# Performance work log

Measured on AMD Instinct MI355X. Metric: run time of the kernel, lower is better.

The kernel has to match this reference:

```python
import jax, jax.numpy as jnp
import numpy as np

B, L_TEXT, N_TOKEN = 8, 2048, 2048
C_TEXT, C_OUT = 3584, 384
C_HID = C_OUT * 2
CHAIN_TYPES = (1, 2)   # heavy, light
CDR_TYPES = (2, 4, 6)  # CDR1/2/3


def setup_inputs() -> dict:
    key = jax.random.key(0)
    ks = jax.random.split(key, 10)
    text_conditioning = jax.random.normal(ks[0], (B, L_TEXT, C_TEXT), jnp.float32)
    text_mask = jnp.ones((B, L_TEXT), jnp.int32)
    chain_type_ids = jax.random.randint(ks[1], (B, L_TEXT), 0, 3).astype(jnp.int32)
    cdr_region_type_ids = jax.random.randint(ks[2], (B, L_TEXT), 0, 10).astype(jnp.int32)
    boltz_chain_type = jax.random.randint(ks[3], (B, N_TOKEN), 0, 4).astype(jnp.int32)
    boltz_region_type = jax.random.randint(ks[4], (B, N_TOKEN), 0, 10).astype(jnp.int32)
    W1 = jax.random.normal(ks[5], (C_HID, C_TEXT), jnp.float32) * 0.02
    b1 = jnp.zeros((C_HID,), jnp.float32)
    W2 = jax.random.normal(ks[6], (C_OUT, C_HID), jnp.float32) * 0.02
    b2 = jnp.zeros((C_OUT,), jnp.float32)
    scale = jnp.ones((1,), jnp.float32)
    return {
        "text_conditioning": text_conditioning, "text_mask": text_mask,
        "chain_type_ids": chain_type_ids, "cdr_region_type_ids": cdr_region_type_ids,
        "boltz_chain_type": boltz_chain_type, "boltz_region_type": boltz_region_type,
        "W1": W1, "b1": b1, "W2": W2, "b2": b2, "scale": scale,
    }


def _align_one(text_proj, tmask, pmask):
    # text_proj: [L, C]; tmask: [L] bool (text CDR positions); pmask: [N] bool (protein CDR positions)
    # The k-th masked text token (in sequence order) maps to the k-th masked protein token,
    # for k < min(n_text, n_protein). Other protein positions get zeros.
    L = tmask.shape[0]
    trank = jnp.cumsum(tmask) - 1          # rank among text CDR tokens
    n_text = jnp.sum(tmask)
    prank = jnp.cumsum(pmask) - 1          # rank among protein CDR tokens
    # idx_by_rank[r] = text index whose rank is r; out-of-range scatter indices dropped
    idx_by_rank = jnp.zeros((L,), jnp.int32).at[jnp.where(tmask, trank, L)].set(
        jnp.arange(L, dtype=jnp.int32), mode="drop")
    valid = pmask & (prank < n_text)       # prank < n_protein holds by construction under pmask
    src = idx_by_rank[jnp.clip(prank, 0, L - 1)]
    emb = text_proj[src]                   # [N, C]
    return jnp.where(valid[:, None], emb, jnp.zeros((), text_proj.dtype))


def reference(text_conditioning, text_mask, chain_type_ids, cdr_region_type_ids,
              boltz_chain_type, boltz_region_type, W1, b1, W2, b2, scale):
    # 2-layer MLP projection: c_text -> 2*c_out -> c_out with SiLU
    h = jax.nn.silu(jnp.einsum("blt,ht->blh", text_conditioning, W1) + b1)
    text_proj = jnp.einsum("blh,ch->blc", h, W2) + b2    # [B, L, C_OUT]

    tm = text_mask.astype(bool)
    result = jnp.zeros((text_conditioning.shape[0], boltz_chain_type.shape[1], W2.shape[0]),
                       text_proj.dtype)
    align = jax.vmap(_align_one)
    for ct in CHAIN_TYPES:
        for rt in CDR_TYPES:
            tmask = (chain_type_ids == ct) & (cdr_region_type_ids == rt) & tm
            pmask = (boltz_chain_type == ct) & (boltz_region_type == rt)
            # (chain, cdr) pairs write to disjoint protein positions, so add is exact
            result = result + align(text_proj, tmask, pmask)
    return scale * result
```

## Files before the change

### kernel.cpp

```cpp
#include <hip/hip_runtime.h>
#include <hip/hip_bf16.h>
#include <math.h>

typedef __bf16 bf16_t;
typedef bf16_t bf16x8 __attribute__((ext_vector_type(8)));
typedef bf16_t bf16x4 __attribute__((ext_vector_type(4)));
typedef float f32x4 __attribute__((ext_vector_type(4)));

#define L_TEXT 2048
#define N_TOKEN 2048
#define C_TEXT 3584
#define C_OUT 384
#define C_HID 768
#define BATCH 8
#define MAXROWS (BATCH * N_TOKEN)
#define PM 3072
#define NPAIR (BATCH * 6)
#define KSPLIT 4
#define KCHUNK (C_TEXT / KSPLIT)

#define NW1 (C_HID * C_TEXT / 8)
#define NW2 (C_OUT * C_HID / 8)
#define NZERO (MAXROWS * C_OUT / 4)
#define CHUNKS_TOTAL (NW1 + NW2 + NZERO)
#define CHUNK_BLOCKS (CHUNKS_TOTAL / 256)
#define GCH (C_TEXT / 8)

__global__ __launch_bounds__(256) void init_map_kernel(
    const float* __restrict__ W1, const float* __restrict__ W2,
    bf16_t* __restrict__ W1b, bf16_t* __restrict__ W2b,
    float* __restrict__ outp,
    const int* __restrict__ tm, const int* __restrict__ ctid,
    const int* __restrict__ cdrid, const int* __restrict__ bct,
    const int* __restrict__ brt,
    int* __restrict__ trowL, int* __restrict__ pidxL, int* __restrict__ vcnt) {
    if (blockIdx.x >= CHUNK_BLOCKS) {
        const int bp = blockIdx.x - CHUNK_BLOCKS;
        const int lane = threadIdx.x;
        if (lane >= 64) return;
        const int b = bp / 6, p = bp % 6;
        const int ct = (p < 3) ? 1 : 2;
        const int rt = 2 + 2 * (p % 3);
        const unsigned long long ltm = (1ull << lane) - 1ull;

        unsigned int tbits = 0, pbits = 0;
#pragma unroll
        for (int i = 0; i < 32; i++) {
            int l = i * 64 + lane;
            unsigned int m = (ctid[b * L_TEXT + l] == ct) &&
                             (cdrid[b * L_TEXT + l] == rt) &&
                             (tm[b * L_TEXT + l] != 0);
            tbits |= m << i;
        }
#pragma unroll
        for (int i = 0; i < 32; i++) {
            int n = i * 64 + lane;
            unsigned int m = (bct[b * N_TOKEN + n] == ct) &&
                             (brt[b * N_TOKEN + n] == rt);
            pbits |= m << i;
        }
        int base = 0;
#pragma unroll
        for (int i = 0; i < 32; i++) {
            bool m = (tbits >> i) & 1;
            unsigned long long bal = __ballot(m);
            if (m) trowL[bp * L_TEXT + base + __popcll(bal & ltm)] = i * 64 + lane;
            base += __popcll(bal);
        }
        const int n_text = base;
        base = 0;
#pragma unroll
        for (int i = 0; i < 32; i++) {
            bool m = (pbits >> i) & 1;
            unsigned long long bal = __ballot(m);
            if (m) pidxL[bp * L_TEXT + base + __popcll(bal & ltm)] = i * 64 + lane;
            base += __popcll(bal);
        }
        const int n_prot = base;
        if (lane == 0) vcnt[bp] = n_text < n_prot ? n_text : n_prot;
        return;
    }
    int idx = blockIdx.x * 256 + threadIdx.x;
    if (idx < NW1) {
        int i = idx * 8;
        float4 v0 = *(const float4*)(W1 + i);
        float4 v1 = *(const float4*)(W1 + i + 4);
        bf16x8 o;
        o[0] = (bf16_t)v0.x; o[1] = (bf16_t)v0.y; o[2] = (bf16_t)v0.z; o[3] = (bf16_t)v0.w;
        o[4] = (bf16_t)v1.x; o[5] = (bf16_t)v1.y; o[6] = (bf16_t)v1.z; o[7] = (bf16_t)v1.w;
        *(bf16x8*)(W1b + i) = o;
    } else if (idx < NW1 + NW2) {
        int i = (idx - NW1) * 8;
        float4 v0 = *(const float4*)(W2 + i);
        float4 v1 = *(const float4*)(W2 + i + 4);
        bf16x8 o;
        o[0] = (bf16_t)v0.x; o[1] = (bf16_t)v0.y; o[2] = (bf16_t)v0.z; o[3] = (bf16_t)v0.w;
        o[4] = (bf16_t)v1.x; o[5] = (bf16_t)v1.y; o[6] = (bf16_t)v1.z; o[7] = (bf16_t)v1.w;
        *(bf16x8*)(W2b + i) = o;
    } else {
        int z = idx - NW1 - NW2;
        f32x4 zv = (f32x4){0.f, 0.f, 0.f, 0.f};
        *(f32x4*)(outp + (size_t)z * 4) = zv;
    }
}

__global__ __launch_bounds__(64) void map_write_kernel(
    const int* __restrict__ trowL, const int* __restrict__ pidxL,
    const int* __restrict__ vcnt,
    int* __restrict__ rows_src, int* __restrict__ rows_dst,
    int* __restrict__ count) {
    const int bp = blockIdx.x;
    const int b = bp / 6;
    const int lane = threadIdx.x;
    int base = 0, total = 0;
    for (int q = 0; q < NPAIR; q++) {
        int v = vcnt[q];
        if (q < bp) base += v;
        total += v;
    }
    if (bp == 0 && lane == 0) *count = total < PM ? total : PM;
    const int v = vcnt[bp];
    for (int r = lane; r < v; r += 64) {
        int g = base + r;
        if (g < PM) {
            rows_src[g] = b * L_TEXT + trowL[bp * L_TEXT + r];
            rows_dst[g] = b * N_TOKEN + pidxL[bp * L_TEXT + r];
        }
    }
}

__global__ __launch_bounds__(256) void gather_kernel(
    const float* __restrict__ X, const int* __restrict__ rows_src,
    const int* __restrict__ countp, bf16_t* __restrict__ Xg) {
    int count = *countp; if (count > PM) count = PM;
    int idx = blockIdx.x * 256 + threadIdx.x;
    int m = idx / GCH;
    if (m >= count) return;
    int c = (idx % GCH) * 8;
    const float* src = X + (size_t)rows_src[m] * C_TEXT + c;
    float4 v0 = *(const float4*)(src);
    float4 v1 = *(const float4*)(src + 4);
    bf16x8 o;
    o[0] = (bf16_t)v0.x; o[1] = (bf16_t)v0.y; o[2] = (bf16_t)v0.z; o[3] = (bf16_t)v0.w;
    o[4] = (bf16_t)v1.x; o[5] = (bf16_t)v1.y; o[6] = (bf16_t)v1.z; o[7] = (bf16_t)v1.w;
    *(bf16x8*)(Xg + (size_t)m * C_TEXT + c) = o;
}

__global__ __launch_bounds__(256) void gemm1_kernel(
    const bf16_t* __restrict__ Xg, const bf16_t* __restrict__ W1b,
    const int* __restrict__ countp, float* __restrict__ P) {
    int count = *countp; if (count > PM) count = PM;
    const int m0 = blockIdx.x * 128;
    if (m0 >= count) return;
    const int n0 = blockIdx.y * 128;
    const int kbeg = blockIdx.z * KCHUNK;

    __shared__ __align__(16) bf16_t As[2][128][40];
    __shared__ __align__(16) bf16_t Bs[2][128][40];

    const int t = threadIdx.x;
    const int lane = t & 63;
    const int w = t >> 6;
    const int wr = w >> 1, wc = w & 1;
    const int fr = lane & 15;
    const int kq = (lane >> 4) * 8;

    f32x4 acc[4][4];
#pragma unroll
    for (int i = 0; i < 4; i++)
#pragma unroll
        for (int j = 0; j < 4; j++) acc[i][j] = (f32x4){0.f, 0.f, 0.f, 0.f};

    const bf16_t* ap[2];
    const bf16_t* bp[2];
    int ofs[2];
#pragma unroll
    for (int j = 0; j < 2; j++) {
        int c = t + 256 * j;
        int row = c >> 2, c8 = (c & 3) * 8;
        ap[j] = Xg + (size_t)(m0 + row) * C_TEXT + kbeg + c8;
        bp[j] = W1b + (size_t)(n0 + row) * C_TEXT + kbeg + c8;
        ofs[j] = row * 40 + c8;
    }

    bf16_t* AsF = &As[0][0][0];
    bf16_t* BsF = &Bs[0][0][0];
    const int BUF = 128 * 40;

    bf16x8 ra[2], rb[2];
#pragma unroll
    for (int j = 0; j < 2; j++) { ra[j] = *(const bf16x8*)(ap[j]); rb[j] = *(const bf16x8*)(bp[j]); }

    const int T = KCHUNK / 32;
    for (int tile = 0; tile < T; ++tile) {
        const int cur = tile & 1;
#pragma unroll
        for (int j = 0; j < 2; j++) {
            *(bf16x8*)(AsF + cur * BUF + ofs[j]) = ra[j];
            *(bf16x8*)(BsF + cur * BUF + ofs[j]) = rb[j];
        }
        bf16x8 na[2], nb[2];
        bool more = (tile + 1 < T);
        if (more) {
            int k = (tile + 1) * 32;
#pragma unroll
            for (int j = 0; j < 2; j++) {
                na[j] = *(const bf16x8*)(ap[j] + k);
                nb[j] = *(const bf16x8*)(bp[j] + k);
            }
        }
        __syncthreads();
        bf16x8 af[4], bfr[4];
#pragma unroll
        for (int mi = 0; mi < 4; mi++)
            af[mi] = *(const bf16x8*)(AsF + cur * BUF + (wr * 64 + mi * 16 + fr) * 40 + kq);
#pragma unroll
        for (int ni = 0; ni < 4; ni++)
            bfr[ni] = *(const bf16x8*)(BsF + cur * BUF + (wc * 64 + ni * 16 + fr) * 40 + kq);
#pragma unroll
        for (int mi = 0; mi < 4; mi++)
#pragma unroll
            for (int ni = 0; ni < 4; ni++)
                acc[mi][ni] = __builtin_amdgcn_mfma_f32_16x16x32_bf16(
                    af[mi], bfr[ni], acc[mi][ni], 0, 0, 0);
        if (more) {
#pragma unroll
            for (int j = 0; j < 2; j++) { ra[j] = na[j]; rb[j] = nb[j]; }
        }
    }

    float* Pk = P + (size_t)blockIdx.z * PM * C_HID;
    const int rj = (lane >> 4) * 4;
#pragma unroll
    for (int mi = 0; mi < 4; mi++) {
#pragma unroll
        for (int ni = 0; ni < 4; ni++) {
            int gn = n0 + wc * 64 + ni * 16 + fr;
#pragma unroll
            for (int j = 0; j < 4; j++) {
                int gm = m0 + wr * 64 + mi * 16 + rj + j;
                if (gm < count) Pk[(size_t)gm * C_HID + gn] = acc[mi][ni][j];
            }
        }
    }
}

__global__ __launch_bounds__(256) void reduce1_kernel(
    const float* __restrict__ P, const float* __restrict__ b1,
    const int* __restrict__ countp, bf16_t* __restrict__ H) {
    int count = *countp; if (count > PM) count = PM;
    int idx = blockIdx.x * 256 + threadIdx.x;
    int m = idx / (C_HID / 4);
    int c = (idx % (C_HID / 4)) * 4;
    if (m >= count) return;
    f32x4 s = *(const f32x4*)(P + (size_t)m * C_HID + c);
#pragma unroll
    for (int ks = 1; ks < KSPLIT; ks++)
        s += *(const f32x4*)(P + ((size_t)ks * PM + m) * C_HID + c);
    f32x4 bb = *(const f32x4*)(b1 + c);
    bf16x4 o;
#pragma unroll
    for (int j = 0; j < 4; j++) {
        float v = s[j] + bb[j];
        o[j] = (bf16_t)(v / (1.0f + __expf(-v)));
    }
    *(bf16x4*)(H + (size_t)m * C_HID + c) = o;
}

__global__ __launch_bounds__(256) void gemm2_kernel(
    const bf16_t* __restrict__ Hm, const bf16_t* __restrict__ W2b,
    const float* __restrict__ b2, const int* __restrict__ rows_dst,
    const int* __restrict__ countp, const float* __restrict__ scale,
    float* __restrict__ outp) {
    int count = *countp; if (count > PM) count = PM;
    const int m0 = blockIdx.x * 32;
    if (m0 >= count) return;
    const int n0 = blockIdx.y * 128;

    __shared__ __align__(16) bf16_t As[2][32][40];
    __shared__ __align__(16) bf16_t Bs[2][128][40];

    const int t = threadIdx.x;
    const int lane = t & 63;
    const int w = t >> 6;
    const int fr = lane & 15;
    const int kq = (lane >> 4) * 8;

    f32x4 acc[2][2];
#pragma unroll
    for (int i = 0; i < 2; i++)
#pragma unroll
        for (int j = 0; j < 2; j++) acc[i][j] = (f32x4){0.f, 0.f, 0.f, 0.f};

    const int arow = t >> 2, ac8 = (t & 3) * 8;
    const bool astage = (t < 128);
    const bf16_t* ap = Hm + (size_t)(m0 + arow) * C_HID + ac8;
    const int aofs = arow * 40 + ac8;
    const bf16_t* bp[2];
    int bofs[2];
#pragma unroll
    for (int j = 0; j < 2; j++) {
        int c = t + 256 * j;
        int row = c >> 2, c8 = (c & 3) * 8;
        bp[j] = W2b + (size_t)(n0 + row) * C_HID + c8;
        bofs[j] = row * 40 + c8;
    }

    bf16_t* AsF = &As[0][0][0];
    bf16_t* BsF = &Bs[0][0][0];
    const int ABUF = 32 * 40, BBUF = 128 * 40;

    bf16x8 ra;
    if (astage) ra = *(const bf16x8*)(ap);
    bf16x8 rb0 = *(const bf16x8*)(bp[0]);
    bf16x8 rb1 = *(const bf16x8*)(bp[1]);

    const int T = C_HID / 32;
    for (int tile = 0; tile < T; ++tile) {
        const int cur = tile & 1;
        if (astage) *(bf16x8*)(AsF + cur * ABUF + aofs) = ra;
        *(bf16x8*)(BsF + cur * BBUF + bofs[0]) = rb0;
        *(bf16x8*)(BsF + cur * BBUF + bofs[1]) = rb1;
        bf16x8 na, nb0, nb1;
        bool more = (tile + 1 < T);
        if (more) {
            int k = (tile + 1) * 32;
            if (astage) na = *(const bf16x8*)(ap + k);
            nb0 = *(const bf16x8*)(bp[0] + k);
            nb1 = *(const bf16x8*)(bp[1] + k);
        }
        __syncthreads();
        bf16x8 af[2], bfr[2];
#pragma unroll
        for (int mi = 0; mi < 2; mi++)
            af[mi] = *(const bf16x8*)(AsF + cur * ABUF + (mi * 16 + fr) * 40 + kq);
#pragma unroll
        for (int ni = 0; ni < 2; ni++)
            bfr[ni] = *(const bf16x8*)(BsF + cur * BBUF + (w * 32 + ni * 16 + fr) * 40 + kq);
#pragma unroll
        for (int mi = 0; mi < 2; mi++)
#pragma unroll
            for (int ni = 0; ni < 2; ni++)
                acc[mi][ni] = __builtin_amdgcn_mfma_f32_16x16x32_bf16(
                    af[mi], bfr[ni], acc[mi][ni], 0, 0, 0);
        if (more) { if (astage) ra = na; rb0 = nb0; rb1 = nb1; }
        __syncthreads();
    }

    const float sc = scale[0];
    const int rj = (lane >> 4) * 4;
#pragma unroll
    for (int mi = 0; mi < 2; mi++) {
#pragma unroll
        for (int ni = 0; ni < 2; ni++) {
            int gn = n0 + w * 32 + ni * 16 + fr;
            float bias = b2[gn];
#pragma unroll
            for (int j = 0; j < 4; j++) {
                int gm = m0 + mi * 16 + rj + j;
                if (gm < count) {
                    int dst = rows_dst[gm];
                    outp[(size_t)dst * C_OUT + gn] = sc * (acc[mi][ni][j] + bias);
                }
            }
        }
    }
}

extern "C" void kernel_launch(void* const* d_in, const int* in_sizes, int n_in,
                              void* d_out, int out_size, void* d_ws, size_t ws_size,
                              hipStream_t stream) {
    const float* X     = (const float*)d_in[0];
    const int*   tm    = (const int*)d_in[1];
    const int*   ctid  = (const int*)d_in[2];
    const int*   cdrid = (const int*)d_in[3];
    const int*   bct   = (const int*)d_in[4];
    const int*   brt   = (const int*)d_in[5];
    const float* W1    = (const float*)d_in[6];
    const float* b1    = (const float*)d_in[7];
    const float* W2    = (const float*)d_in[8];
    const float* b2    = (const float*)d_in[9];
    const float* scale = (const float*)d_in[10];

    char* ws = (char*)d_ws;
    size_t off = 0;
    int* count = (int*)(ws + off);        off += 1024;
    int* vcnt = (int*)(ws + off);         off += 1024;
    int* rows_src = (int*)(ws + off);     off += (size_t)PM * 4;
    int* rows_dst = (int*)(ws + off);     off += (size_t)PM * 4;
    int* trowL = (int*)(ws + off);        off += (size_t)NPAIR * L_TEXT * 4;
    int* pidxL = (int*)(ws + off);        off += (size_t)NPAIR * L_TEXT * 4;
    bf16_t* W1b = (bf16_t*)(ws + off);    off += (size_t)C_HID * C_TEXT * 2;
    bf16_t* W2b = (bf16_t*)(ws + off);    off += (size_t)C_OUT * C_HID * 2;
    bf16_t* Xg = (bf16_t*)(ws + off);     off += (size_t)PM * C_TEXT * 2;
    bf16_t* H = (bf16_t*)(ws + off);      off += (size_t)PM * C_HID * 2;
    float* P = (float*)(ws + off);        off += (size_t)KSPLIT * PM * C_HID * 4;
    float* outp = (float*)d_out;

    init_map_kernel<<<CHUNK_BLOCKS + NPAIR, 256, 0, stream>>>(
        W1, W2, W1b, W2b, outp, tm, ctid, cdrid, bct, brt, trowL, pidxL, vcnt);

    map_write_kernel<<<NPAIR, 64, 0, stream>>>(trowL, pidxL, vcnt,
                                               rows_src, rows_dst, count);

    gather_kernel<<<(PM * GCH) / 256, 256, 0, stream>>>(X, rows_src, count, Xg);

    dim3 g1(PM / 128, C_HID / 128, KSPLIT);
    gemm1_kernel<<<g1, 256, 0, stream>>>(Xg, W1b, count, P);

    reduce1_kernel<<<(PM * C_HID / 4) / 256, 256, 0, stream>>>(P, b1, count, H);

    dim3 g2(PM / 32, C_OUT / 128);
    gemm2_kernel<<<g2, 256, 0, stream>>>(H, W2b, b2, rows_dst, count, scale, outp);
}
```

Baseline: 124.8 us.

## Load GEMM1 tiles directly into LDS with global_load_lds

Replaces the register-staged, double-buffered LDS tile loading in gemm1 with direct global-to-LDS 16-byte loads into a single unpadded buffer. This drops the register round trip and the LDS store instructions. In exchange it loses the prefetch overlap, adds a second barrier per k-tile, and removes the padding, so LDS bank conflicts may rise on the fragment reads.

```diff
diff --git a/kernel.cpp b/kernel.cpp
--- a/kernel.cpp
+++ b/kernel.cpp
@@ -25,6 +25,12 @@
 #define CHUNKS_TOTAL (NW1 + NW2 + NZERO)
 #define CHUNK_BLOCKS (CHUNKS_TOTAL / 256)
 #define GCH (C_TEXT / 8)
+
+__device__ __forceinline__ void gload16(const bf16_t* g, bf16_t* l) {
+    __builtin_amdgcn_global_load_lds(
+        (const __attribute__((address_space(1))) void*)g,
+        (__attribute__((address_space(3))) void*)l, 16, 0, 0);
+}
 
 __global__ __launch_bounds__(256) void init_map_kernel(
     const float* __restrict__ W1, const float* __restrict__ W2,
@@ -155,8 +161,8 @@
     const int n0 = blockIdx.y * 128;
     const int kbeg = blockIdx.z * KCHUNK;
 
-    __shared__ __align__(16) bf16_t As[2][128][40];
-    __shared__ __align__(16) bf16_t Bs[2][128][40];
+    __shared__ __align__(1024) bf16_t As[128][32];
+    __shared__ __align__(1024) bf16_t Bs[128][32];
 
     const int t = threadIdx.x;
     const int lane = t & 63;
@@ -171,62 +177,45 @@
 #pragma unroll
         for (int j = 0; j < 4; j++) acc[i][j] = (f32x4){0.f, 0.f, 0.f, 0.f};
 
-    const bf16_t* ap[2];
-    const bf16_t* bp[2];
-    int ofs[2];
+    const int lr = lane >> 2;
+    const int lc8 = (lane & 3) * 8;
+    const bf16_t* aptr[2];
+    const bf16_t* bptr[2];
+    bf16_t* alds[2];
+    bf16_t* blds[2];
 #pragma unroll
     for (int j = 0; j < 2; j++) {
-        int c = t + 256 * j;
-        int row = c >> 2, c8 = (c & 3) * 8;
-        ap[j] = Xg + (size_t)(m0 + row) * C_TEXT + kbeg + c8;
-        bp[j] = W1b + (size_t)(n0 + row) * C_TEXT + kbeg + c8;
-        ofs[j] = row * 40 + c8;
-    }
-
-    bf16_t* AsF = &As[0][0][0];
-    bf16_t* BsF = &Bs[0][0][0];
-    const int BUF = 128 * 40;
-
-    bf16x8 ra[2], rb[2];
-#pragma unroll
-    for (int j = 0; j < 2; j++) { ra[j] = *(const bf16x8*)(ap[j]); rb[j] = *(const bf16x8*)(bp[j]); }
+        int q = w * 2 + j;
+        int row = q * 16 + lr;
+        aptr[j] = Xg + (size_t)(m0 + row) * C_TEXT + kbeg + lc8;
+        bptr[j] = W1b + (size_t)(n0 + row) * C_TEXT + kbeg + lc8;
+        alds[j] = &As[q * 16][0];
+        blds[j] = &Bs[q * 16][0];
+    }
 
     const int T = KCHUNK / 32;
     for (int tile = 0; tile < T; ++tile) {
-        const int cur = tile & 1;
+        const int kt = tile * 32;
 #pragma unroll
         for (int j = 0; j < 2; j++) {
-            *(bf16x8*)(AsF + cur * BUF + ofs[j]) = ra[j];
-            *(bf16x8*)(BsF + cur * BUF + ofs[j]) = rb[j];
-        }
-        bf16x8 na[2], nb[2];
-        bool more = (tile + 1 < T);
-        if (more) {
-            int k = (tile + 1) * 32;
-#pragma unroll
-            for (int j = 0; j < 2; j++) {
-                na[j] = *(const bf16x8*)(ap[j] + k);
-                nb[j] = *(const bf16x8*)(bp[j] + k);
-            }
+            gload16(aptr[j] + kt, alds[j]);
+            gload16(bptr[j] + kt, blds[j]);
         }
         __syncthreads();
         bf16x8 af[4], bfr[4];
 #pragma unroll
         for (int mi = 0; mi < 4; mi++)
-            af[mi] = *(const bf16x8*)(AsF + cur * BUF + (wr * 64 + mi * 16 + fr) * 40 + kq);
+            af[mi] = *(const bf16x8*)&As[wr * 64 + mi * 16 + fr][kq];
 #pragma unroll
         for (int ni = 0; ni < 4; ni++)
-            bfr[ni] = *(const bf16x8*)(BsF + cur * BUF + (wc * 64 + ni * 16 + fr) * 40 + kq);
+            bfr[ni] = *(const bf16x8*)&Bs[wc * 64 + ni * 16 + fr][kq];
 #pragma unroll
         for (int mi = 0; mi < 4; mi++)
 #pragma unroll
             for (int ni = 0; ni < 4; ni++)
                 acc[mi][ni] = __builtin_amdgcn_mfma_f32_16x16x32_bf16(
                     af[mi], bfr[ni], acc[mi][ni], 0, 0, 0);
-        if (more) {
-#pragma unroll
-            for (int j = 0; j < 2; j++) { ra[j] = na[j]; rb[j] = nb[j]; }
-        }
+        __syncthreads();
     }
 
     float* Pk = P + (size_t)blockIdx.z * PM * C_HID;
```

Result: slower. 137.1 us (+9.9%).
